# Optimization experiments

Hardware: AMD Instinct MI355X
Metric: run time of the kernel (lower is better)

Reference implementation:

```python
import jax, jax.numpy as jnp
import numpy as np

B, N, T, D, H, E = 2, 1024, 8, 128, 4, 8192
DH = D // H
NEG_SLOPE = 0.2  # GATv2Conv default negative_slope


def _ln(x, g, b):
    m = jnp.mean(x, -1, keepdims=True)
    v = jnp.mean((x - m) ** 2, -1, keepdims=True)
    return (x - m) * jax.lax.rsqrt(v + 1e-5) * g + b


def _forward(x, edge_index, gat_wl, gat_wr, gat_att, gat_b, in_w, in_b, out_w, out_b,
             ffn_w1, ffn_b1, ffn_w2, ffn_b2, fus_w, fus_b,
             lns_g, lns_b, lnt1_g, lnt1_b, lnt2_g, lnt2_b, lnf_g, lnf_b):
    # ---- spatial branch: GATv2, vectorized over (B, T) instead of python loops ----
    loops = jnp.arange(N)
    src = jnp.concatenate([edge_index[0], loops])  # j: message source (PyG adds self loops)
    dst = jnp.concatenate([edge_index[1], loops])  # i: aggregation target
    xl = jnp.einsum('bntd,de->bnte', x, gat_wl).reshape(B, N, T, H, D)
    xr = jnp.einsum('bntd,de->bnte', x, gat_wr).reshape(B, N, T, H, D)
    ml = xl[:, src]                                  # [B,Et,T,H,D]
    mr = xr[:, dst]
    e = jax.nn.leaky_relu(ml + mr, NEG_SLOPE)
    logits = jnp.einsum('bethd,hd->beth', e, gat_att)
    logits = jnp.moveaxis(logits, 1, 0)              # [Et,B,T,H]
    mx = jax.ops.segment_max(logits, dst, num_segments=N)
    p = jnp.exp(logits - mx[dst])                    # stable edge softmax per dst node
    ssum = jax.ops.segment_sum(p, dst, num_segments=N)
    alpha = p / ssum[dst]                            # [Et,B,T,H]
    msg = alpha[..., None] * jnp.moveaxis(ml, 1, 0)
    agg = jax.ops.segment_sum(msg, dst, num_segments=N)  # [N,B,T,H,D]
    x_sp = jnp.moveaxis(agg.mean(3), 0, 1) + gat_b   # concat=False -> head mean; [B,N,T,D]
    x_sp = _ln(x_sp, lns_g, lns_b)

    # ---- temporal branch: MHA + FFN, vectorized over all B*N nodes ----
    xt = x.reshape(B * N, T, D)
    qkv = xt @ in_w + in_b
    q, k, v = jnp.split(qkv, 3, axis=-1)
    q = q.reshape(B * N, T, H, DH)
    k = k.reshape(B * N, T, H, DH)
    v = v.reshape(B * N, T, H, DH)
    scores = jnp.einsum('bthd,bshd->bhts', q, k) / np.float32(np.sqrt(DH))
    attn = jax.nn.softmax(scores, -1)
    o = jnp.einsum('bhts,bshd->bthd', attn, v).reshape(B * N, T, D)
    o = o @ out_w + out_b
    x1 = _ln(xt + o, lnt1_g, lnt1_b)
    ffn = jax.nn.gelu(x1 @ ffn_w1 + ffn_b1, approximate=False) @ ffn_w2 + ffn_b2
    x_tp = _ln(x1 + ffn, lnt2_g, lnt2_b).reshape(B, N, T, D)

    # ---- gated fusion with residual ----
    g = jax.nn.sigmoid(jnp.concatenate([x_sp, x_tp], -1) @ fus_w + fus_b)
    return _ln(g * x_sp + (1.0 - g) * x_tp + x, lnf_g, lnf_b)


def setup_inputs() -> dict:
    key = jax.random.key(0)
    ks = jax.random.split(key, 12)
    s = 0.05
    f = jnp.float32
    return {
        'x': jax.random.normal(ks[0], (B, N, T, D), f),
        'edge_index': jax.random.randint(ks[1], (2, E), 0, N),
        'gat_wl': jax.random.normal(ks[2], (D, H * D), f) * s,
        'gat_wr': jax.random.normal(ks[3], (D, H * D), f) * s,
        'gat_att': jax.random.normal(ks[4], (H, D), f) * s,
        'gat_b': jnp.zeros((D,), f),
        'in_w': jax.random.normal(ks[5], (D, 3 * D), f) * s,
        'in_b': jnp.zeros((3 * D,), f),
        'out_w': jax.random.normal(ks[6], (D, D), f) * s,
        'out_b': jnp.zeros((D,), f),
        'ffn_w1': jax.random.normal(ks[7], (D, 4 * D), f) * s,
        'ffn_b1': jnp.zeros((4 * D,), f),
        'ffn_w2': jax.random.normal(ks[8], (4 * D, D), f) * s,
        'ffn_b2': jnp.zeros((D,), f),
        'fus_w': jax.random.normal(ks[9], (2 * D, D), f) * s,
        'fus_b': jnp.zeros((D,), f),
        'lns_g': jnp.ones((D,), f), 'lns_b': jnp.zeros((D,), f),
        'lnt1_g': jnp.ones((D,), f), 'lnt1_b': jnp.zeros((D,), f),
        'lnt2_g': jnp.ones((D,), f), 'lnt2_b': jnp.zeros((D,), f),
        'lnf_g': jnp.ones((D,), f), 'lnf_b': jnp.zeros((D,), f),
    }


def reference(x, edge_index, gat_wl, gat_wr, gat_att, gat_b, in_w, in_b, out_w, out_b,
              ffn_w1, ffn_b1, ffn_w2, ffn_b2, fus_w, fus_b,
              lns_g, lns_b, lnt1_g, lnt1_b, lnt2_g, lnt2_b, lnf_g, lnf_b):
    return _forward(x, edge_index, gat_wl, gat_wr, gat_att, gat_b, in_w, in_b, out_w, out_b,
                    ffn_w1, ffn_b1, ffn_w2, ffn_b2, fus_w, fus_b,
                    lns_g, lns_b, lnt1_g, lnt1_b, lnt2_g, lnt2_b, lnf_g, lnf_b)
```

## Files before the change

kernel.cpp:

```cpp
#include <hip/hip_runtime.h>
#include <math.h>

#define B_ 2
#define N_ 1024
#define T_ 8
#define D_ 128
#define H_ 4
#define E_ 8192
#define EN_ 9216
#define M_ 16384

typedef unsigned short u16;
using bf16x8 = __attribute__((ext_vector_type(8))) short;
using f32x4  = __attribute__((ext_vector_type(4))) float;

__device__ __forceinline__ float bf2f(unsigned int u) {
  return __uint_as_float(u << 16);
}
__device__ __forceinline__ u16 f2bf(float f) {
  unsigned int x = __float_as_uint(f);
  x += 0x7fffu + ((x >> 16) & 1u);
  return (u16)(x >> 16);
}
__device__ __forceinline__ void load8f(const u16* p, float* f) {
  uint4 u = *(const uint4*)p;
  f[0]=bf2f(u.x & 0xffffu); f[1]=bf2f(u.x >> 16);
  f[2]=bf2f(u.y & 0xffffu); f[3]=bf2f(u.y >> 16);
  f[4]=bf2f(u.z & 0xffffu); f[5]=bf2f(u.z >> 16);
  f[6]=bf2f(u.w & 0xffffu); f[7]=bf2f(u.w >> 16);
}
__device__ __forceinline__ void unpack8(uint4 u, float* f) {
  f[0]=bf2f(u.x & 0xffffu); f[1]=bf2f(u.x >> 16);
  f[2]=bf2f(u.y & 0xffffu); f[3]=bf2f(u.y >> 16);
  f[4]=bf2f(u.z & 0xffffu); f[5]=bf2f(u.z >> 16);
  f[6]=bf2f(u.w & 0xffffu); f[7]=bf2f(u.w >> 16);
}
__device__ __forceinline__ void gl2lds(const u16* g, u16* l) {
  __builtin_amdgcn_global_load_lds(
      (const __attribute__((address_space(1))) unsigned int*)(const void*)g,
      (__attribute__((address_space(3))) unsigned int*)(void*)l,
      16, 0, 0);
}

__device__ __forceinline__ u16 conv_w_elem(int idx,
    const float* wl, const float* wr, const float* inw, const float* outw,
    const float* f1, const float* f2, const float* fw) {
  const float* src; int base, K, N;
  if      (idx < 65536)  { src = wl;   base = 0;      K = 128; N = 512; }
  else if (idx < 131072) { src = wr;   base = 65536;  K = 128; N = 512; }
  else if (idx < 180224) { src = inw;  base = 131072; K = 128; N = 384; }
  else if (idx < 196608) { src = outw; base = 180224; K = 128; N = 128; }
  else if (idx < 262144) { src = f1;   base = 196608; K = 128; N = 512; }
  else if (idx < 327680) { src = f2;   base = 262144; K = 512; N = 128; }
  else                   { src = fw;   base = 327680; K = 256; N = 128; }
  int o = idx - base;
  int n = o / K, k = o - n * K;
  return f2bf(src[k * N + n]);
}

__global__ __launch_bounds__(1024) void prep_csr_k(const float* __restrict__ x,
    const float* __restrict__ wl, const float* __restrict__ wr,
    const float* __restrict__ inw, const float* __restrict__ outw,
    const float* __restrict__ f1, const float* __restrict__ f2,
    const float* __restrict__ fw,
    u16* __restrict__ XB, u16* __restrict__ WB,
    const int* __restrict__ ei, int* __restrict__ offs, int* __restrict__ srcs) {
  __shared__ int cnt[N_];
  __shared__ int cur[N_];
  int bi = blockIdx.x;
  int tid = threadIdx.x;
  if (bi < 512) {
    int i = (bi * 1024 + tid) * 4;
    float4 v = *(const float4*)&x[i];
    u16 o[4] = {f2bf(v.x), f2bf(v.y), f2bf(v.z), f2bf(v.w)};
    *(ushort4*)&XB[i] = *(ushort4*)o;
    return;
  }
  if (bi < 600) {
    int base = (bi - 512) * 4096 + tid * 4;
#pragma unroll
    for (int j = 0; j < 4; ++j)
      WB[base + j] = conv_w_elem(base + j, wl, wr, inw, outw, f1, f2, fw);
    return;
  }
  cnt[tid] = 0;
  __syncthreads();
  for (int e = tid; e < EN_; e += 1024) {
    int d = (e < E_) ? ei[E_ + e] : (e - E_);
    atomicAdd(&cnt[d], 1);
  }
  __syncthreads();
  int mine = cnt[tid];
  for (int off = 1; off < 1024; off <<= 1) {
    int tv = (tid >= off) ? cnt[tid - off] : 0;
    __syncthreads();
    cnt[tid] += tv;
    __syncthreads();
  }
  int excl = cnt[tid] - mine;
  offs[tid] = excl;
  if (tid == 1023) offs[N_] = cnt[1023];
  cur[tid] = excl;
  __syncthreads();
  for (int e = tid; e < EN_; e += 1024) {
    int d = (e < E_) ? ei[E_ + e] : (e - E_);
    int s = (e < E_) ? ei[e] : (e - E_);
    int pos = atomicAdd(&cur[d], 1);
    srcs[pos] = s;
  }
}

template<int BM, int ACT, int ROUTE>
__device__ __forceinline__ void gemm_tile(int bx, int by,
    const u16* A, int lda, const u16* WT, int K, const float* bias,
    u16* C, int ldc, u16* R0, u16* R1, u16* R2, const float* b2,
    u16* As, u16* Bs) {
  constexpr int MI = BM / 32;
  int tid = threadIdx.x;
  int lane = tid & 63, wid = tid >> 6;
  int lr = lane & 15, lk = lane >> 4;
  int wm = (wid >> 1) * (BM / 2);
  int wn = (wid & 1) * 64;

  u16* Cb; int ldc_; int col0; const float* bias_;
  if (ROUTE) {
    if (bx < 4)      { Cb = R0; ldc_ = 512; col0 = bx * 128;       bias_ = nullptr; }
    else if (bx < 8) { Cb = R1; ldc_ = 512; col0 = (bx - 4) * 128; bias_ = nullptr; }
    else             { Cb = R2; ldc_ = 384; col0 = (bx - 8) * 128; bias_ = b2; }
  } else { Cb = C; ldc_ = ldc; col0 = bx * 128; bias_ = bias; }

  f32x4 acc[MI][4] = {};
  for (int k0 = 0; k0 < K; k0 += 32) {
    __syncthreads();
#pragma unroll
    for (int i = 0; i < BM / 64; ++i) {
      int o = tid * 16 + i * 4096;
      int row = o >> 6;
      int col = (o >> 1) & 31;
      gl2lds(A + (size_t)(by * BM + row) * lda + k0 + col,
             (u16*)((char*)As + wid * 1024 + i * 4096));
    }
#pragma unroll
    for (int i = 0; i < 2; ++i) {
      int o = tid * 16 + i * 4096;
      int nrow = o >> 6;
      int col = (o >> 1) & 31;
      gl2lds(WT + (size_t)(bx * 128 + nrow) * K + k0 + col,
             (u16*)((char*)Bs + wid * 1024 + i * 4096));
    }
    __syncthreads();
    bf16x8 bf[4];
#pragma unroll
    for (int ni = 0; ni < 4; ++ni)
      bf[ni] = *(const bf16x8*)&Bs[(wn + ni * 16 + lr) * 32 + lk * 8];
#pragma unroll
    for (int mi = 0; mi < MI; ++mi) {
      bf16x8 af = *(const bf16x8*)&As[(wm + mi * 16 + lr) * 32 + lk * 8];
#pragma unroll
      for (int ni = 0; ni < 4; ++ni)
        acc[mi][ni] = __builtin_amdgcn_mfma_f32_16x16x32_bf16(af, bf[ni], acc[mi][ni], 0, 0, 0);
    }
  }
  float bc[4];
#pragma unroll
  for (int ni = 0; ni < 4; ++ni)
    bc[ni] = bias_ ? bias_[col0 + wn + ni * 16 + lr] : 0.f;
#pragma unroll
  for (int mi = 0; mi < MI; ++mi) {
#pragma unroll
    for (int r = 0; r < 4; ++r) {
      int row = by * BM + wm + mi * 16 + lk * 4 + r;
#pragma unroll
      for (int ni = 0; ni < 4; ++ni) {
        int col = col0 + wn + ni * 16 + lr;
        float v = acc[mi][ni][r] + bc[ni];
        if (ACT) v = 0.5f * v * (1.f + erff(v * 0.70710678118f));
        Cb[(size_t)row * ldc_ + col] = f2bf(v);
      }
    }
  }
}

template<int EPI>
__device__ __forceinline__ void ln_epilogue(int by, f32x4 (&acc)[2][4],
    const float* bias, const float* xres, const u16* xcat,
    const float* lng, const float* lnb,
    float* o32, u16* o16, int os16, float* rs, float* rq) {
  int tid = threadIdx.x;
  int lane = tid & 63, wid = tid >> 6;
  int lr = lane & 15, lk = lane >> 4;
  int wm = (wid >> 1) * 32, wn = (wid & 1) * 64;
  float bc[4];
#pragma unroll
  for (int ni = 0; ni < 4; ++ni) bc[ni] = bias[wn + ni * 16 + lr];
#pragma unroll
  for (int mi = 0; mi < 2; ++mi) {
#pragma unroll
    for (int r = 0; r < 4; ++r) {
      int row = by * 64 + wm + mi * 16 + lk * 4 + r;
      float s = 0.f, s2 = 0.f;
#pragma unroll
      for (int ni = 0; ni < 4; ++ni) {
        int col = wn + ni * 16 + lr;
        float v = acc[mi][ni][r] + bc[ni];
        if (EPI == 1 || EPI == 2) {
          v += xres[(size_t)row * 128 + col];
        } else {
          float gg = 1.f / (1.f + __expf(-v));
          float xsp = bf2f(xcat[(size_t)row * 256 + col]);
          float xtp = bf2f(xcat[(size_t)row * 256 + 128 + col]);
          v = gg * xsp + (1.f - gg) * xtp + xres[(size_t)row * 128 + col];
        }
        acc[mi][ni][r] = v;
        s += v; s2 += v * v;
      }
      s += __shfl_xor(s, 1, 64); s2 += __shfl_xor(s2, 1, 64);
      s += __shfl_xor(s, 2, 64); s2 += __shfl_xor(s2, 2, 64);
      s += __shfl_xor(s, 4, 64); s2 += __shfl_xor(s2, 4, 64);
      s += __shfl_xor(s, 8, 64); s2 += __shfl_xor(s2, 8, 64);
      if (lr == 0) {
        int rl = wm + mi * 16 + lk * 4 + r;
        rs[rl * 2 + (wid & 1)] = s;
        rq[rl * 2 + (wid & 1)] = s2;
      }
    }
  }
  __syncthreads();
#pragma unroll
  for (int mi = 0; mi < 2; ++mi) {
#pragma unroll
    for (int r = 0; r < 4; ++r) {
      int rl = wm + mi * 16 + lk * 4 + r;
      int row = by * 64 + rl;
      float tot = rs[rl * 2] + rs[rl * 2 + 1];
      float tq = rq[rl * 2] + rq[rl * 2 + 1];
      float mean = tot * (1.f / 128.f);
      float var = tq * (1.f / 128.f) - mean * mean;
      float rinv = rsqrtf(var + 1e-5f);
#pragma unroll
      for (int ni = 0; ni < 4; ++ni) {
        int col = wn + ni * 16 + lr;
        float o = (acc[mi][ni][r] - mean) * rinv * lng[col] + lnb[col];
        if (EPI != 2) o32[(size_t)row * 128 + col] = o;
        if (EPI != 3) o16[(size_t)row * os16 + col] = f2bf(o);
      }
    }
  }
}

template<int EPI>
__global__ __launch_bounds__(256) void gemm_ln_k(const u16* __restrict__ A, int lda,
    const u16* __restrict__ WT, int K, const float* __restrict__ bias,
    const float* __restrict__ xres, const u16* __restrict__ xcat,
    const float* __restrict__ lng, const float* __restrict__ lnb,
    float* __restrict__ o32, u16* __restrict__ o16, int os16) {
  __shared__ u16 As[64 * 32];
  __shared__ u16 Bs[128 * 32];
  __shared__ float rs[128], rq[128];
  int by = blockIdx.x;
  int tid = threadIdx.x;
  int lane = tid & 63, wid = tid >> 6;
  int lr = lane & 15, lk = lane >> 4;
  int wm = (wid >> 1) * 32, wn = (wid & 1) * 64;

  f32x4 acc[2][4] = {};
  for (int k0 = 0; k0 < K; k0 += 32) {
    __syncthreads();
    {
      int o = tid * 16;
      int row = o >> 6;
      int col = (o >> 1) & 31;
      gl2lds(A + (size_t)(by * 64 + row) * lda + k0 + col,
             (u16*)((char*)As + wid * 1024));
    }
#pragma unroll
    for (int i = 0; i < 2; ++i) {
      int o = tid * 16 + i * 4096;
      int nrow = o >> 6;
      int col = (o >> 1) & 31;
      gl2lds(WT + (size_t)nrow * K + k0 + col,
             (u16*)((char*)Bs + wid * 1024 + i * 4096));
    }
    __syncthreads();
    bf16x8 bf[4];
#pragma unroll
    for (int ni = 0; ni < 4; ++ni)
      bf[ni] = *(const bf16x8*)&Bs[(wn + ni * 16 + lr) * 32 + lk * 8];
#pragma unroll
    for (int mi = 0; mi < 2; ++mi) {
      bf16x8 af = *(const bf16x8*)&As[(wm + mi * 16 + lr) * 32 + lk * 8];
#pragma unroll
      for (int ni = 0; ni < 4; ++ni)
        acc[mi][ni] = __builtin_amdgcn_mfma_f32_16x16x32_bf16(af, bf[ni], acc[mi][ni], 0, 0, 0);
    }
  }
  ln_epilogue<EPI>(by, acc, bias, xres, xcat, lng, lnb, o32, o16, os16, rs, rq);
}

__global__ __launch_bounds__(256) void proj_k(const u16* __restrict__ XB,
    const u16* __restrict__ WT1, const float* __restrict__ in_b,
    u16* __restrict__ XL, u16* __restrict__ XR, u16* __restrict__ QKV) {
  __shared__ u16 As[128 * 32];
  __shared__ u16 Bs[128 * 32];
  gemm_tile<128, 0, 1>(blockIdx.x, blockIdx.y, XB, 128, WT1, 128, nullptr,
                       nullptr, 0, XL, XR, QKV, in_b, As, Bs);
}

__global__ __launch_bounds__(256) void attn_oproj_k(const u16* __restrict__ QKV,
    const u16* __restrict__ WTO, const float* __restrict__ out_b,
    const float* __restrict__ x,
    const float* __restrict__ lnt1_g, const float* __restrict__ lnt1_b,
    float* __restrict__ X1, u16* __restrict__ X1B) {
  __shared__ u16 As[4 * 64 * 32];
  __shared__ u16 Bs[4 * 128 * 32];
  __shared__ float rs[128], rq[128];
  int by = blockIdx.x;
  int tid = threadIdx.x;
  int lane = tid & 63, wid = tid >> 6;

#pragma unroll
  for (int i = 0; i < 8; ++i) {
    int o = tid * 16 + i * 4096;
    int c = o >> 13;
    int wb = o & 8191;
    int nrow = wb >> 6;
    int kin = (wb & 63) >> 1;
    gl2lds(WTO + (size_t)nrow * 128 + c * 32 + kin,
           (u16*)((char*)Bs + wid * 1024 + i * 4096));
  }

  int t = lane >> 3, sidx = lane & 7, dg = lane & 7;
  for (int it = 0; it < 8; ++it) {
    int task = wid * 8 + it;
    int bnl = task >> 2, h = task & 3;
    int bn = by * 8 + bnl;
    const u16* base = QKV + (size_t)bn * 8 * 384;
    float va[8][4];
#pragma unroll
    for (int s2 = 0; s2 < 8; ++s2) {
      ushort4 vv = *(const ushort4*)(base + s2 * 384 + 256 + h * 32 + dg * 4);
      va[s2][0] = bf2f(vv.x); va[s2][1] = bf2f(vv.y);
      va[s2][2] = bf2f(vv.z); va[s2][3] = bf2f(vv.w);
    }
    const u16* qp = base + t * 384 + h * 32;
    const u16* kp = base + sidx * 384 + 128 + h * 32;
    float sc = 0.f;
#pragma unroll
    for (int d0 = 0; d0 < 32; d0 += 8) {
      float q[8], k[8];
      load8f(qp + d0, q);
      load8f(kp + d0, k);
#pragma unroll
      for (int j = 0; j < 8; ++j) sc += q[j] * k[j];
    }
    sc *= 0.17677669529663687f;
    float m = sc;
    m = fmaxf(m, __shfl_xor(m, 1, 64));
    m = fmaxf(m, __shfl_xor(m, 2, 64));
    m = fmaxf(m, __shfl_xor(m, 4, 64));
    float p = __expf(sc - m);
    float S = p;
    S += __shfl_xor(S, 1, 64);
    S += __shfl_xor(S, 2, 64);
    S += __shfl_xor(S, 4, 64);
    float alpha = p / S;
    int tb = lane & 56;
    float o0 = 0.f, o1 = 0.f, o2 = 0.f, o3 = 0.f;
#pragma unroll
    for (int s2 = 0; s2 < 8; ++s2) {
      float a = __shfl(alpha, tb + s2, 64);
      o0 += a * va[s2][0];
      o1 += a * va[s2][1];
      o2 += a * va[s2][2];
      o3 += a * va[s2][3];
    }
    u16 ov[4] = {f2bf(o0), f2bf(o1), f2bf(o2), f2bf(o3)};
    int row = bnl * 8 + t;
    *(ushort4*)&As[h * 2048 + row * 32 + dg * 4] = *(ushort4*)ov;
  }
  __syncthreads();

  int lr = lane & 15, lk = lane >> 4;
  int wm = (wid >> 1) * 32, wn = (wid & 1) * 64;
  f32x4 acc[2][4] = {};
#pragma unroll
  for (int c = 0; c < 4; ++c) {
    bf16x8 bf[4];
#pragma unroll
    for (int ni = 0; ni < 4; ++ni)
      bf[ni] = *(const bf16x8*)&Bs[c * 4096 + (wn + ni * 16 + lr) * 32 + lk * 8];
#pragma unroll
    for (int mi = 0; mi < 2; ++mi) {
      bf16x8 af = *(const bf16x8*)&As[c * 2048 + (wm + mi * 16 + lr) * 32 + lk * 8];
#pragma unroll
      for (int ni = 0; ni < 4; ++ni)
        acc[mi][ni] = __builtin_amdgcn_mfma_f32_16x16x32_bf16(af, bf[ni], acc[mi][ni], 0, 0, 0);
    }
  }
  ln_epilogue<1>(by, acc, out_b, x, nullptr, lnt1_g, lnt1_b, X1, X1B, 128, rs, rq);
}

__device__ __forceinline__ void gat_wave(int w, int lane,
    const u16* XL, const u16* XR, const int* offs, const int* srcs,
    const float* att, const float* gb, const float* lng, const float* lnb,
    u16* XCAT) {
  int n = w >> 4;
  int b = (w >> 3) & 1;
  int t = w & 7;
  int dd = (lane & 15) * 8;
  size_t tokn = (size_t)(b * N_ + n) * 8 + t;
  size_t rowoff = (size_t)b * (N_ * 8) + t;

  float mr[8], av[8];
  load8f(XR + tokn * 512 + lane * 8, mr);
  *(float4*)&av[0] = *(const float4*)(att + lane * 8);
  *(float4*)&av[4] = *(const float4*)(att + lane * 8 + 4);

  int beg = offs[n], end = offs[n + 1];
  float sH = 0.f;
  float acc[8] = {0.f, 0.f, 0.f, 0.f, 0.f, 0.f, 0.f, 0.f};
  int src0 = srcs[beg];
  uint4 raw_next = *(const uint4*)(XL + (rowoff + (size_t)src0 * 8) * 512 + lane * 8);
  for (int i = beg; i < end; ++i) {
    uint4 raw = raw_next;
    if (i + 1 < end) {
      int sn = srcs[i + 1];
      raw_next = *(const uint4*)(XL + (rowoff + (size_t)sn * 8) * 512 + lane * 8);
    }
    float ml[8];
    unpack8(raw, ml);
    float d = 0.f;
#pragma unroll
    for (int j = 0; j < 8; ++j) {
      float m = ml[j] + mr[j];
      m = fmaxf(m, 0.2f * m);
      d += m * av[j];
    }
    d += __shfl_xor(d, 1, 64);
    d += __shfl_xor(d, 2, 64);
    d += __shfl_xor(d, 4, 64);
    d += __shfl_xor(d, 8, 64);
    float p = __expf(d);
    sH += p;
#pragma unroll
    for (int j = 0; j < 8; ++j) acc[j] += p * ml[j];
  }
  float invS = 1.f / sH;
#pragma unroll
  for (int j = 0; j < 8; ++j) acc[j] *= invS;
#pragma unroll
  for (int j = 0; j < 8; ++j) {
    acc[j] += __shfl_xor(acc[j], 16, 64);
    acc[j] += __shfl_xor(acc[j], 32, 64);
  }
#pragma unroll
  for (int j = 0; j < 8; ++j) acc[j] = acc[j] * 0.25f + gb[dd + j];
  float s = 0.f, s2 = 0.f;
#pragma unroll
  for (int j = 0; j < 8; ++j) { s += acc[j]; s2 += acc[j] * acc[j]; }
#pragma unroll
  for (int m = 1; m < 16; m <<= 1) {
    s += __shfl_xor(s, m, 64);
    s2 += __shfl_xor(s2, m, 64);
  }
  float mean = s * (1.f / 128.f);
  float var = s2 * (1.f / 128.f) - mean * mean;
  float r = rsqrtf(var + 1e-5f);
  if (lane < 16) {
    u16 ob[8];
#pragma unroll
    for (int j = 0; j < 8; ++j)
      ob[j] = f2bf((acc[j] - mean) * r * lng[dd + j] + lnb[dd + j]);
    *(uint4*)&XCAT[tokn * 256 + dd] = *(uint4*)ob;
  }
}

__global__ __launch_bounds__(256) void ffn1_gat_k(const u16* __restrict__ X1B,
    const u16* __restrict__ WTF1, const float* __restrict__ ffn_b1,
    u16* __restrict__ FFNH,
    const u16* __restrict__ XL, const u16* __restrict__ XR,
    const int* __restrict__ offs, const int* __restrict__ srcs,
    const float* __restrict__ att, const float* __restrict__ gb,
    const float* __restrict__ lng, const float* __restrict__ lnb,
    u16* __restrict__ XCAT) {
  __shared__ u16 As[128 * 32];
  __shared__ u16 Bs[128 * 32];
  int bid = blockIdx.x;
  if (bid < 512) {
    gemm_tile<128, 1, 0>(bid >> 7, bid & 127, X1B, 128, WTF1, 128, ffn_b1,
                         FFNH, 512, nullptr, nullptr, nullptr, nullptr, As, Bs);
  } else {
    gat_wave((bid - 512) * 4 + (threadIdx.x >> 6), threadIdx.x & 63,
             XL, XR, offs, srcs, att, gb, lng, lnb, XCAT);
  }
}

extern "C" void kernel_launch(void* const* d_in, const int* in_sizes, int n_in,
                              void* d_out, int out_size, void* d_ws, size_t ws_size,
                              hipStream_t stream) {
  const float* x       = (const float*)d_in[0];
  const int*   ei      = (const int*)d_in[1];
  const float* gat_att = (const float*)d_in[4];
  const float* gat_b   = (const float*)d_in[5];
  const float* in_b    = (const float*)d_in[7];
  const float* out_b   = (const float*)d_in[9];
  const float* ffn_b1  = (const float*)d_in[11];
  const float* ffn_b2  = (const float*)d_in[13];
  const float* fus_b   = (const float*)d_in[15];
  const float* lns_g   = (const float*)d_in[16];
  const float* lns_b   = (const float*)d_in[17];
  const float* lnt1_g  = (const float*)d_in[18];
  const float* lnt1_b  = (const float*)d_in[19];
  const float* lnt2_g  = (const float*)d_in[20];
  const float* lnt2_b  = (const float*)d_in[21];
  const float* lnf_g   = (const float*)d_in[22];
  const float* lnf_b   = (const float*)d_in[23];

  char* ws = (char*)d_ws;
  u16*   WB    = (u16*)ws;
  u16*   WTO   = WB + 180224;
  u16*   WTF1  = WB + 196608;
  u16*   WTF2  = WB + 262144;
  u16*   WTFUS = WB + 327680;
  int*   OFFS  = (int*)(ws + 3145728);
  int*   SRCS  = (int*)(ws + 3153920);
  u16*   XB   = (u16*)(ws + 4194304);
  u16*   XL   = (u16*)(ws + 8388608);
  u16*   XR   = (u16*)(ws + 25165824);
  float* X1   = (float*)(ws + 41943040);
  u16*   QKV  = (u16*)(ws + 50331648);
  u16*   X1B  = (u16*)(ws + 62914560);
  u16*   FFNH = (u16*)(ws + 67108864);
  u16*   XCAT = (u16*)(ws + 83886080);

  prep_csr_k<<<dim3(601), dim3(1024), 0, stream>>>(x,
      (const float*)d_in[2], (const float*)d_in[3], (const float*)d_in[6],
      (const float*)d_in[8], (const float*)d_in[10], (const float*)d_in[12],
      (const float*)d_in[14], XB, WB, ei, OFFS, SRCS);

  proj_k<<<dim3(11, 128), dim3(256), 0, stream>>>(XB, WB, in_b, XL, XR, QKV);

  attn_oproj_k<<<dim3(256), dim3(256), 0, stream>>>(QKV, WTO, out_b, x,
      lnt1_g, lnt1_b, X1, X1B);

  ffn1_gat_k<<<dim3(4608), dim3(256), 0, stream>>>(X1B, WTF1, ffn_b1, FFNH,
      XL, XR, OFFS, SRCS, gat_att, gat_b, lns_g, lns_b, XCAT);

  gemm_ln_k<2><<<dim3(256), dim3(256), 0, stream>>>(FFNH, 512, WTF2, 512,
      ffn_b2, X1, nullptr, lnt2_g, lnt2_b, nullptr, XCAT + 128, 256);

  gemm_ln_k<3><<<dim3(256), dim3(256), 0, stream>>>(XCAT, 256, WTFUS, 256,
      fus_b, x, XCAT, lnf_g, lnf_b, (float*)d_out, nullptr, 0);
}
```

Before: 228.5 us.

## Fuse FFN1+GELU+FFN2+LN per row block and co-schedule GAT with attention

```diff
diff --git a/kernel.cpp b/kernel.cpp
--- a/kernel.cpp
+++ b/kernel.cpp
@@ -248,12 +248,11 @@
   }
 }
 
-template<int EPI>
-__global__ __launch_bounds__(256) void gemm_ln_k(const u16* __restrict__ A, int lda,
-    const u16* __restrict__ WT, int K, const float* __restrict__ bias,
+__global__ __launch_bounds__(256) void fusion_k(const u16* __restrict__ A,
+    const u16* __restrict__ WT, const float* __restrict__ bias,
     const float* __restrict__ xres, const u16* __restrict__ xcat,
     const float* __restrict__ lng, const float* __restrict__ lnb,
-    float* __restrict__ o32, u16* __restrict__ o16, int os16) {
+    float* __restrict__ o32) {
   __shared__ u16 As[64 * 32];
   __shared__ u16 Bs[128 * 32];
   __shared__ float rs[128], rq[128];
@@ -262,6 +261,7 @@
   int lane = tid & 63, wid = tid >> 6;
   int lr = lane & 15, lk = lane >> 4;
   int wm = (wid >> 1) * 32, wn = (wid & 1) * 64;
+  const int K = 256;
 
   f32x4 acc[2][4] = {};
   for (int k0 = 0; k0 < K; k0 += 32) {
@@ -270,7 +270,7 @@
       int o = tid * 16;
       int row = o >> 6;
       int col = (o >> 1) & 31;
-      gl2lds(A + (size_t)(by * 64 + row) * lda + k0 + col,
+      gl2lds(A + (size_t)(by * 64 + row) * K + k0 + col,
              (u16*)((char*)As + wid * 1024));
     }
 #pragma unroll
@@ -294,7 +294,7 @@
         acc[mi][ni] = __builtin_amdgcn_mfma_f32_16x16x32_bf16(af, bf[ni], acc[mi][ni], 0, 0, 0);
     }
   }
-  ln_epilogue<EPI>(by, acc, bias, xres, xcat, lng, lnb, o32, o16, os16, rs, rq);
+  ln_epilogue<3>(by, acc, bias, xres, xcat, lng, lnb, o32, nullptr, 0, rs, rq);
 }
 
 __global__ __launch_bounds__(256) void proj_k(const u16* __restrict__ XB,
@@ -306,29 +306,139 @@
                        nullptr, 0, XL, XR, QKV, in_b, As, Bs);
 }
 
-__global__ __launch_bounds__(256) void attn_oproj_k(const u16* __restrict__ QKV,
+__device__ __forceinline__ void gat_wave(int w, int lane,
+    const u16* XL, const u16* XR, const int* offs, const int* srcs,
+    const float* att, const float* gb, const float* lng, const float* lnb,
+    u16* XCAT) {
+  int n = w >> 4;
+  int b = (w >> 3) & 1;
+  int t = w & 7;
+  int dd = (lane & 15) * 8;
+  size_t tokn = (size_t)(b * N_ + n) * 8 + t;
+  size_t rowoff = (size_t)b * (N_ * 8) + t;
+
+  float mr[8], av[8];
+  load8f(XR + tokn * 512 + lane * 8, mr);
+  *(float4*)&av[0] = *(const float4*)(att + lane * 8);
+  *(float4*)&av[4] = *(const float4*)(att + lane * 8 + 4);
+
+  int beg = offs[n], end = offs[n + 1];
+  float sH = 0.f;
+  float acc[8] = {0.f, 0.f, 0.f, 0.f, 0.f, 0.f, 0.f, 0.f};
+  int i = beg;
+  uint4 r0 = *(const uint4*)(XL + (rowoff + (size_t)srcs[i] * 8) * 512 + lane * 8);
+  uint4 r1 = r0;
+  if (i + 1 < end)
+    r1 = *(const uint4*)(XL + (rowoff + (size_t)srcs[i + 1] * 8) * 512 + lane * 8);
+  while (i + 1 < end) {
+    uint4 c0 = r0, c1 = r1;
+    if (i + 2 < end)
+      r0 = *(const uint4*)(XL + (rowoff + (size_t)srcs[i + 2] * 8) * 512 + lane * 8);
+    if (i + 3 < end)
+      r1 = *(const uint4*)(XL + (rowoff + (size_t)srcs[i + 3] * 8) * 512 + lane * 8);
+    float ml0[8], ml1[8];
+    unpack8(c0, ml0);
+    unpack8(c1, ml1);
+    float d0 = 0.f, d1 = 0.f;
+#pragma unroll
+    for (int j = 0; j < 8; ++j) {
+      float m0 = ml0[j] + mr[j];
+      m0 = fmaxf(m0, 0.2f * m0);
+      d0 += m0 * av[j];
+      float m1 = ml1[j] + mr[j];
+      m1 = fmaxf(m1, 0.2f * m1);
+      d1 += m1 * av[j];
+    }
+    d0 += __shfl_xor(d0, 1, 64); d1 += __shfl_xor(d1, 1, 64);
+    d0 += __shfl_xor(d0, 2, 64); d1 += __shfl_xor(d1, 2, 64);
+    d0 += __shfl_xor(d0, 4, 64); d1 += __shfl_xor(d1, 4, 64);
+    d0 += __shfl_xor(d0, 8, 64); d1 += __shfl_xor(d1, 8, 64);
+    float p0 = __expf(d0), p1 = __expf(d1);
+    sH += p0 + p1;
+#pragma unroll
+    for (int j = 0; j < 8; ++j) acc[j] += p0 * ml0[j] + p1 * ml1[j];
+    i += 2;
+  }
+  if (i < end) {
+    float ml0[8];
+    unpack8(r0, ml0);
+    float d0 = 0.f;
+#pragma unroll
+    for (int j = 0; j < 8; ++j) {
+      float m0 = ml0[j] + mr[j];
+      m0 = fmaxf(m0, 0.2f * m0);
+      d0 += m0 * av[j];
+    }
+    d0 += __shfl_xor(d0, 1, 64);
+    d0 += __shfl_xor(d0, 2, 64);
+    d0 += __shfl_xor(d0, 4, 64);
+    d0 += __shfl_xor(d0, 8, 64);
+    float p0 = __expf(d0);
+    sH += p0;
+#pragma unroll
+    for (int j = 0; j < 8; ++j) acc[j] += p0 * ml0[j];
+  }
+  float invS = 1.f / sH;
+#pragma unroll
+  for (int j = 0; j < 8; ++j) acc[j] *= invS;
+#pragma unroll
+  for (int j = 0; j < 8; ++j) {
+    acc[j] += __shfl_xor(acc[j], 16, 64);
+    acc[j] += __shfl_xor(acc[j], 32, 64);
+  }
+#pragma unroll
+  for (int j = 0; j < 8; ++j) acc[j] = acc[j] * 0.25f + gb[dd + j];
+  float s = 0.f, s2 = 0.f;
+#pragma unroll
+  for (int j = 0; j < 8; ++j) { s += acc[j]; s2 += acc[j] * acc[j]; }
+#pragma unroll
+  for (int m = 1; m < 16; m <<= 1) {
+    s += __shfl_xor(s, m, 64);
+    s2 += __shfl_xor(s2, m, 64);
+  }
+  float mean = s * (1.f / 128.f);
+  float var = s2 * (1.f / 128.f) - mean * mean;
+  float r = rsqrtf(var + 1e-5f);
+  if (lane < 16) {
+    u16 ob[8];
+#pragma unroll
+    for (int j = 0; j < 8; ++j)
+      ob[j] = f2bf((acc[j] - mean) * r * lng[dd + j] + lnb[dd + j]);
+    *(uint4*)&XCAT[tokn * 256 + dd] = *(uint4*)ob;
+  }
+}
+
+__global__ __launch_bounds__(256) void attn_gat_k(const u16* __restrict__ QKV,
     const u16* __restrict__ WTO, const float* __restrict__ out_b,
     const float* __restrict__ x,
     const float* __restrict__ lnt1_g, const float* __restrict__ lnt1_b,
-    float* __restrict__ X1, u16* __restrict__ X1B) {
+    float* __restrict__ X1, u16* __restrict__ X1B,
+    const u16* __restrict__ XL, const u16* __restrict__ XR,
+    const int* __restrict__ offs, const int* __restrict__ srcs,
+    const float* __restrict__ att, const float* __restrict__ gb,
+    const float* __restrict__ lns_g, const float* __restrict__ lns_b,
+    u16* __restrict__ XCAT) {
   __shared__ u16 As[4 * 64 * 32];
-  __shared__ u16 Bs[4 * 128 * 32];
+  __shared__ u16 Bs[2 * 128 * 32];
   __shared__ float rs[128], rq[128];
-  int by = blockIdx.x;
+  int bid = blockIdx.x;
   int tid = threadIdx.x;
   int lane = tid & 63, wid = tid >> 6;
 
-#pragma unroll
-  for (int i = 0; i < 8; ++i) {
-    int o = tid * 16 + i * 4096;
-    int c = o >> 13;
-    int wb = o & 8191;
-    int nrow = wb >> 6;
-    int kin = (wb & 63) >> 1;
-    gl2lds(WTO + (size_t)nrow * 128 + c * 32 + kin,
-           (u16*)((char*)Bs + wid * 1024 + i * 4096));
-  }
-
+  if (bid >= 256) {
+    gat_wave((bid - 256) * 4 + wid, lane, XL, XR, offs, srcs,
+             att, gb, lns_g, lns_b, XCAT);
+    return;
+  }
+  int by = bid;
+  {
+    int o = tid * 16;
+    gl2lds(WTO + (size_t)(o >> 6) * 128 + ((o >> 1) & 31),
+           (u16*)((char*)Bs + wid * 1024));
+    o = tid * 16 + 4096;
+    gl2lds(WTO + (size_t)(o >> 6) * 128 + ((o >> 1) & 31),
+           (u16*)((char*)Bs + 4096 + wid * 1024));
+  }
   int t = lane >> 3, sidx = lane & 7, dg = lane & 7;
   for (int it = 0; it < 8; ++it) {
     int task = wid * 8 + it;
@@ -378,121 +488,123 @@
     int row = bnl * 8 + t;
     *(ushort4*)&As[h * 2048 + row * 32 + dg * 4] = *(ushort4*)ov;
   }
-  __syncthreads();
-
   int lr = lane & 15, lk = lane >> 4;
   int wm = (wid >> 1) * 32, wn = (wid & 1) * 64;
   f32x4 acc[2][4] = {};
-#pragma unroll
-  for (int c = 0; c < 4; ++c) {
+  for (int kc = 0; kc < 4; ++kc) {
+    __syncthreads();
+    if (kc < 3) {
+      char* dstb = (char*)Bs + ((kc + 1) & 1) * 8192;
+      int o = tid * 16;
+      gl2lds(WTO + (size_t)(o >> 6) * 128 + (kc + 1) * 32 + ((o >> 1) & 31),
+             (u16*)(dstb + wid * 1024));
+      o = tid * 16 + 4096;
+      gl2lds(WTO + (size_t)(o >> 6) * 128 + (kc + 1) * 32 + ((o >> 1) & 31),
+             (u16*)(dstb + 4096 + wid * 1024));
+    }
+    const u16* Bc = Bs + (kc & 1) * 4096;
     bf16x8 bf[4];
 #pragma unroll
     for (int ni = 0; ni < 4; ++ni)
-      bf[ni] = *(const bf16x8*)&Bs[c * 4096 + (wn + ni * 16 + lr) * 32 + lk * 8];
+      bf[ni] = *(const bf16x8*)&Bc[(wn + ni * 16 + lr) * 32 + lk * 8];
 #pragma unroll
     for (int mi = 0; mi < 2; ++mi) {
-      bf16x8 af = *(const bf16x8*)&As[c * 2048 + (wm + mi * 16 + lr) * 32 + lk * 8];
+      bf16x8 af = *(const bf16x8*)&As[kc * 2048 + (wm + mi * 16 + lr) * 32 + lk * 8];
 #pragma unroll
       for (int ni = 0; ni < 4; ++ni)
         acc[mi][ni] = __builtin_amdgcn_mfma_f32_16x16x32_bf16(af, bf[ni], acc[mi][ni], 0, 0, 0);
     }
   }
+  __syncthreads();
   ln_epilogue<1>(by, acc, out_b, x, nullptr, lnt1_g, lnt1_b, X1, X1B, 128, rs, rq);
 }
 
-__device__ __forceinline__ void gat_wave(int w, int lane,
-    const u16* XL, const u16* XR, const int* offs, const int* srcs,
-    const float* att, const float* gb, const float* lng, const float* lnb,
-    u16* XCAT) {
-  int n = w >> 4;
-  int b = (w >> 3) & 1;
-  int t = w & 7;
-  int dd = (lane & 15) * 8;
-  size_t tokn = (size_t)(b * N_ + n) * 8 + t;
-  size_t rowoff = (size_t)b * (N_ * 8) + t;
-
-  float mr[8], av[8];
-  load8f(XR + tokn * 512 + lane * 8, mr);
-  *(float4*)&av[0] = *(const float4*)(att + lane * 8);
-  *(float4*)&av[4] = *(const float4*)(att + lane * 8 + 4);
-
-  int beg = offs[n], end = offs[n + 1];
-  float sH = 0.f;
-  float acc[8] = {0.f, 0.f, 0.f, 0.f, 0.f, 0.f, 0.f, 0.f};
-  int src0 = srcs[beg];
-  uint4 raw_next = *(const uint4*)(XL + (rowoff + (size_t)src0 * 8) * 512 + lane * 8);
-  for (int i = beg; i < end; ++i) {
-    uint4 raw = raw_next;
-    if (i + 1 < end) {
-      int sn = srcs[i + 1];
-      raw_next = *(const uint4*)(XL + (rowoff + (size_t)sn * 8) * 512 + lane * 8);
-    }
-    float ml[8];
-    unpack8(raw, ml);
-    float d = 0.f;
-#pragma unroll
-    for (int j = 0; j < 8; ++j) {
-      float m = ml[j] + mr[j];
-      m = fmaxf(m, 0.2f * m);
-      d += m * av[j];
-    }
-    d += __shfl_xor(d, 1, 64);
-    d += __shfl_xor(d, 2, 64);
-    d += __shfl_xor(d, 4, 64);
-    d += __shfl_xor(d, 8, 64);
-    float p = __expf(d);
-    sH += p;
-#pragma unroll
-    for (int j = 0; j < 8; ++j) acc[j] += p * ml[j];
-  }
-  float invS = 1.f / sH;
-#pragma unroll
-  for (int j = 0; j < 8; ++j) acc[j] *= invS;
-#pragma unroll
-  for (int j = 0; j < 8; ++j) {
-    acc[j] += __shfl_xor(acc[j], 16, 64);
-    acc[j] += __shfl_xor(acc[j], 32, 64);
-  }
-#pragma unroll
-  for (int j = 0; j < 8; ++j) acc[j] = acc[j] * 0.25f + gb[dd + j];
-  float s = 0.f, s2 = 0.f;
-#pragma unroll
-  for (int j = 0; j < 8; ++j) { s += acc[j]; s2 += acc[j] * acc[j]; }
-#pragma unroll
-  for (int m = 1; m < 16; m <<= 1) {
-    s += __shfl_xor(s, m, 64);
-    s2 += __shfl_xor(s2, m, 64);
-  }
-  float mean = s * (1.f / 128.f);
-  float var = s2 * (1.f / 128.f) - mean * mean;
-  float r = rsqrtf(var + 1e-5f);
-  if (lane < 16) {
-    u16 ob[8];
-#pragma unroll
-    for (int j = 0; j < 8; ++j)
-      ob[j] = f2bf((acc[j] - mean) * r * lng[dd + j] + lnb[dd + j]);
-    *(uint4*)&XCAT[tokn * 256 + dd] = *(uint4*)ob;
-  }
-}
-
-__global__ __launch_bounds__(256) void ffn1_gat_k(const u16* __restrict__ X1B,
-    const u16* __restrict__ WTF1, const float* __restrict__ ffn_b1,
-    u16* __restrict__ FFNH,
-    const u16* __restrict__ XL, const u16* __restrict__ XR,
-    const int* __restrict__ offs, const int* __restrict__ srcs,
-    const float* __restrict__ att, const float* __restrict__ gb,
+__global__ __launch_bounds__(256) void ffn_fused_k(const u16* __restrict__ X1B,
+    const u16* __restrict__ WTF1, const u16* __restrict__ WTF2,
+    const float* __restrict__ b1, const float* __restrict__ b2,
+    const float* __restrict__ X1,
     const float* __restrict__ lng, const float* __restrict__ lnb,
-    u16* __restrict__ XCAT) {
-  __shared__ u16 As[128 * 32];
-  __shared__ u16 Bs[128 * 32];
-  int bid = blockIdx.x;
-  if (bid < 512) {
-    gemm_tile<128, 1, 0>(bid >> 7, bid & 127, X1B, 128, WTF1, 128, ffn_b1,
-                         FFNH, 512, nullptr, nullptr, nullptr, nullptr, As, Bs);
-  } else {
-    gat_wave((bid - 512) * 4 + (threadIdx.x >> 6), threadIdx.x & 63,
-             XL, XR, offs, srcs, att, gb, lng, lnb, XCAT);
-  }
+    u16* __restrict__ XCATr) {
+  __shared__ u16 As[64 * 128];
+  __shared__ u16 B1s[64 * 128];
+  __shared__ u16 B2s[128 * 64];
+  __shared__ u16 Hc[2 * 64 * 40];
+  __shared__ float rs[128], rq[128];
+  int by = blockIdx.x;
+  int tid = threadIdx.x;
+  int lane = tid & 63, wid = tid >> 6;
+  int lr = lane & 15, lk = lane >> 4;
+
+#pragma unroll
+  for (int kc = 0; kc < 4; ++kc) {
+    gl2lds(X1B + (size_t)(by * 64 + (tid >> 2)) * 128 + kc * 32 + (tid & 3) * 8,
+           (u16*)((char*)As + kc * 4096 + wid * 1024));
+  }
+  int wr0 = (wid >> 1) * 32, wc0 = (wid & 1) * 32;
+  int wm = (wid >> 1) * 32, wn = (wid & 1) * 64;
+  f32x4 acc2[2][4] = {};
+  for (int nc = 0; nc < 8; ++nc) {
+    __syncthreads();
+#pragma unroll
+    for (int kc = 0; kc < 4; ++kc) {
+      gl2lds(WTF1 + (size_t)(nc * 64 + (tid >> 2)) * 128 + kc * 32 + (tid & 3) * 8,
+             (u16*)((char*)B1s + kc * 4096 + wid * 1024));
+    }
+#pragma unroll
+    for (int i = 0; i < 4; ++i) {
+      int o = tid * 16 + i * 4096;
+      int kc2l = o >> 13;
+      int wb = o & 8191;
+      int nrow = wb >> 6;
+      int kin = (wb & 63) >> 1;
+      gl2lds(WTF2 + (size_t)nrow * 512 + nc * 64 + kc2l * 32 + kin,
+             (u16*)((char*)B2s + wid * 1024 + i * 4096));
+    }
+    __syncthreads();
+    f32x4 a1[2][2] = {};
+#pragma unroll
+    for (int kc = 0; kc < 4; ++kc) {
+      bf16x8 bf0 = *(const bf16x8*)&B1s[kc * 2048 + (wc0 + lr) * 32 + lk * 8];
+      bf16x8 bf1 = *(const bf16x8*)&B1s[kc * 2048 + (wc0 + 16 + lr) * 32 + lk * 8];
+#pragma unroll
+      for (int mi = 0; mi < 2; ++mi) {
+        bf16x8 af = *(const bf16x8*)&As[kc * 2048 + (wr0 + mi * 16 + lr) * 32 + lk * 8];
+        a1[mi][0] = __builtin_amdgcn_mfma_f32_16x16x32_bf16(af, bf0, a1[mi][0], 0, 0, 0);
+        a1[mi][1] = __builtin_amdgcn_mfma_f32_16x16x32_bf16(af, bf1, a1[mi][1], 0, 0, 0);
+      }
+    }
+#pragma unroll
+    for (int mi = 0; mi < 2; ++mi) {
+#pragma unroll
+      for (int r = 0; r < 4; ++r) {
+        int row = wr0 + mi * 16 + lk * 4 + r;
+#pragma unroll
+        for (int ni = 0; ni < 2; ++ni) {
+          int cl = wc0 + ni * 16 + lr;
+          float v = a1[mi][ni][r] + b1[nc * 64 + cl];
+          v = 0.5f * v * (1.f + erff(v * 0.70710678118f));
+          Hc[(cl >> 5) * 2560 + row * 40 + (cl & 31)] = f2bf(v);
+        }
+      }
+    }
+    __syncthreads();
+#pragma unroll
+    for (int kc2l = 0; kc2l < 2; ++kc2l) {
+      bf16x8 bf[4];
+#pragma unroll
+      for (int ni = 0; ni < 4; ++ni)
+        bf[ni] = *(const bf16x8*)&B2s[kc2l * 4096 + (wn + ni * 16 + lr) * 32 + lk * 8];
+#pragma unroll
+      for (int mi = 0; mi < 2; ++mi) {
+        bf16x8 af = *(const bf16x8*)&Hc[kc2l * 2560 + (wm + mi * 16 + lr) * 40 + lk * 8];
+#pragma unroll
+        for (int ni = 0; ni < 4; ++ni)
+          acc2[mi][ni] = __builtin_amdgcn_mfma_f32_16x16x32_bf16(af, bf[ni], acc2[mi][ni], 0, 0, 0);
+      }
+    }
+  }
+  __syncthreads();
+  ln_epilogue<2>(by, acc2, b2, X1, nullptr, lng, lnb, nullptr, XCATr, 256, rs, rq);
 }
 
 extern "C" void kernel_launch(void* const* d_in, const int* in_sizes, int n_in,
@@ -530,8 +642,7 @@
   float* X1   = (float*)(ws + 41943040);
   u16*   QKV  = (u16*)(ws + 50331648);
   u16*   X1B  = (u16*)(ws + 62914560);
-  u16*   FFNH = (u16*)(ws + 67108864);
-  u16*   XCAT = (u16*)(ws + 83886080);
+  u16*   XCAT = (u16*)(ws + 67108864);
 
   prep_csr_k<<<dim3(601), dim3(1024), 0, stream>>>(x,
       (const float*)d_in[2], (const float*)d_in[3], (const float*)d_in[6],
@@ -540,15 +651,13 @@
 
   proj_k<<<dim3(11, 128), dim3(256), 0, stream>>>(XB, WB, in_b, XL, XR, QKV);
 
-  attn_oproj_k<<<dim3(256), dim3(256), 0, stream>>>(QKV, WTO, out_b, x,
-      lnt1_g, lnt1_b, X1, X1B);
-
-  ffn1_gat_k<<<dim3(4608), dim3(256), 0, stream>>>(X1B, WTF1, ffn_b1, FFNH,
-      XL, XR, OFFS, SRCS, gat_att, gat_b, lns_g, lns_b, XCAT);
-
-  gemm_ln_k<2><<<dim3(256), dim3(256), 0, stream>>>(FFNH, 512, WTF2, 512,
-      ffn_b2, X1, nullptr, lnt2_g, lnt2_b, nullptr, XCAT + 128, 256);
-
-  gemm_ln_k<3><<<dim3(256), dim3(256), 0, stream>>>(XCAT, 256, WTFUS, 256,
-      fus_b, x, XCAT, lnf_g, lnf_b, (float*)d_out, nullptr, 0);
-}
+  attn_gat_k<<<dim3(4352), dim3(256), 0, stream>>>(QKV, WTO, out_b, x,
+      lnt1_g, lnt1_b, X1, X1B, XL, XR, OFFS, SRCS,
+      gat_att, gat_b, lns_g, lns_b, XCAT);
+
+  ffn_fused_k<<<dim3(256), dim3(256), 0, stream>>>(X1B, WTF1, WTF2,
+      ffn_b1, ffn_b2, X1, lnt2_g, lnt2_b, XCAT + 128);
+
+  fusion_k<<<dim3(256), dim3(256), 0, stream>>>(XCAT, WTFUS, fus_b, x, XCAT,
+      lnf_g, lnf_b, (float*)d_out);
+}
```

New measurement: 232.3 us. About the same (+1.7%).
